# Performance work log

Measured on AMD Instinct MI355X. Metric: run time of the kernel, lower is better.

## Reference

```python
import jax, jax.numpy as jnp
import numpy as np

EMBED_DIM = 768
MAX_LEN = 1024
ALPHA = 0.99
BATCH = 16


def setup_inputs() -> dict:
    key = jax.random.key(0)
    k1, k2, k3 = jax.random.split(key, 3)
    x = jax.random.normal(k1, (BATCH, MAX_LEN, EMBED_DIM), dtype=jnp.float32)
    # torch nn.Linear(embed_dim, 3*embed_dim): store weight as [in, out] for x @ W
    scale = 1.0 / np.sqrt(EMBED_DIM)
    W_qkv = jax.random.uniform(k2, (EMBED_DIM, 3 * EMBED_DIM), dtype=jnp.float32,
                               minval=-scale, maxval=scale)
    b_qkv = jax.random.uniform(k3, (3 * EMBED_DIM,), dtype=jnp.float32,
                               minval=-scale, maxval=scale)
    return {"x": x, "W_qkv": W_qkv, "b_qkv": b_qkv}


def _retention_mask(sl, alpha, dtype):
    # M[i, j] = alpha**(i - j) if i >= j else 0 (causal tril * decay)
    i = jnp.arange(sl)[:, None]
    j = jnp.arange(sl)[None, :]
    causal = i >= j
    # compute decay only where causal to avoid huge alpha**(negative) values
    exponent = jnp.where(causal, (i - j).astype(dtype), 0.0)
    decay = jnp.asarray(alpha, dtype) ** exponent
    return jnp.where(causal, decay, jnp.zeros((), dtype))


def reference(x, W_qkv, b_qkv):
    bs, sl, d = x.shape
    qkv = x @ W_qkv + b_qkv                      # [B, S, 3D]
    q, k, v = jnp.split(qkv, 3, axis=-1)         # each [B, S, D]
    M = _retention_mask(sl, ALPHA, x.dtype)      # [S, S]
    scores = jnp.einsum('bsd,btd->bst', q, k) / jnp.sqrt(jnp.asarray(d, x.dtype))
    out = jnp.einsum('bst,btd->bsd', scores * M[None, :, :], v)
    return out
```

## Files before the change

kernel.cpp:

```cpp
#include <hip/hip_runtime.h>
#include <hip/hip_bf16.h>


#define SEQ   1024
#define DIM   768
#define ND3   2304

typedef __attribute__((ext_vector_type(8))) short bf16x8;
typedef __attribute__((ext_vector_type(4))) float f32x4;

#define L2A     (-0.014499569695115089f)
#define RSQRTD  (0.03608439182435161f)

__device__ __forceinline__ unsigned short f2bf(float x) {
  union { float f; unsigned u; } v; v.f = x;
  unsigned r = v.u + 0x7FFFu + ((v.u >> 16) & 1u);
  return (unsigned short)(r >> 16);
}

__device__ __forceinline__ void gload16(const void* g, void* l) {
  __builtin_amdgcn_global_load_lds(
      (const __attribute__((address_space(1))) void*)g,
      (__attribute__((address_space(3))) void*)l, 16, 0, 0);
}

__device__ __forceinline__ void gemm_core(
    const unsigned short* gA, const unsigned short* gA2,
    const unsigned short* gB, const unsigned short* gB2,
    char* lsA, char* lsB, int nt, int wid, int lane, f32x4 acc[2][4]) {
  int lr = lane & 15, lg = lane >> 4;
  int wm = wid >> 1, wn = wid & 1;
  int rdA = (wm * 32 + lr) * 128 + ((lg ^ (lr & 7)) << 4);
  int rdB = (wn * 64 + lr) * 128 + ((lg ^ (lr & 7)) << 4);
  int wo = wid * 2048;

#define STAGE(t, par) do {                                                    \
    int lo_ = ((par) << 14) + wo;                                             \
    gload16(gA  + (size_t)(t) * 64, lsA + lo_);                               \
    gload16(gA2 + (size_t)(t) * 64, lsA + lo_ + 1024);                        \
    gload16(gB  + (size_t)(t) * 64, lsB + lo_);                               \
    gload16(gB2 + (size_t)(t) * 64, lsB + lo_ + 1024);                        \
  } while (0)

  STAGE(0, 0);
  STAGE(1, 1);
  asm volatile("s_waitcnt vmcnt(4)" ::: "memory");
  __builtin_amdgcn_s_barrier();
  asm volatile("" ::: "memory");

  for (int t = 0; t < nt; ++t) {
    int pbase = (t & 1) << 14;
    bf16x8 aF[2][2], bF[2][4];
#pragma unroll
    for (int kh = 0; kh < 2; ++kh) {
#pragma unroll
      for (int f = 0; f < 2; ++f)
        aF[kh][f] = *(const bf16x8*)(lsA + pbase + ((rdA + f * 2048) ^ (kh << 6)));
#pragma unroll
      for (int n = 0; n < 4; ++n)
        bF[kh][n] = *(const bf16x8*)(lsB + pbase + ((rdB + n * 2048) ^ (kh << 6)));
    }
    __builtin_amdgcn_s_setprio(1);
#pragma unroll
    for (int kh = 0; kh < 2; ++kh)
#pragma unroll
      for (int f = 0; f < 2; ++f)
#pragma unroll
        for (int n = 0; n < 4; ++n)
          acc[f][n] = __builtin_amdgcn_mfma_f32_16x16x32_bf16(aF[kh][f], bF[kh][n], acc[f][n], 0, 0, 0);
    __builtin_amdgcn_s_setprio(0);

    if (t == nt - 1) break;
    __builtin_amdgcn_s_barrier();
    asm volatile("" ::: "memory");
    if (t + 2 < nt) {
      STAGE(t + 2, t & 1);
      asm volatile("s_waitcnt vmcnt(4)" ::: "memory");
    } else {
      asm volatile("s_waitcnt vmcnt(0)" ::: "memory");
    }
    __builtin_amdgcn_s_barrier();
    asm volatile("" ::: "memory");
  }
#undef STAGE
}

__global__ void convert_x(const float* __restrict__ x, unsigned short* __restrict__ xb) {
  size_t i = ((size_t)blockIdx.x * 256 + threadIdx.x) * 8;
  float4 f0 = *(const float4*)(x + i);
  float4 f1 = *(const float4*)(x + i + 4);
  bf16x8 v;
  v[0] = (short)f2bf(f0.x); v[1] = (short)f2bf(f0.y);
  v[2] = (short)f2bf(f0.z); v[3] = (short)f2bf(f0.w);
  v[4] = (short)f2bf(f1.x); v[5] = (short)f2bf(f1.y);
  v[6] = (short)f2bf(f1.z); v[7] = (short)f2bf(f1.w);
  *(bf16x8*)(xb + i) = v;
}

__global__ void transpose_w(const float* __restrict__ W, unsigned short* __restrict__ Wt) {
  __shared__ float tile[64][65];
  int n0 = (blockIdx.x % 36) * 64;
  int k0 = (blockIdx.x / 36) * 64;
  int tx = threadIdx.x & 63, ty = threadIdx.x >> 6;
#pragma unroll
  for (int p = 0; p < 16; ++p) {
    int k = ty + p * 4;
    tile[k][tx] = W[(size_t)(k0 + k) * ND3 + n0 + tx];
  }
  __syncthreads();
#pragma unroll
  for (int p = 0; p < 16; ++p) {
    int n = ty + p * 4;
    Wt[(size_t)(n0 + n) * DIM + k0 + tx] = f2bf(tile[tx][n]);
  }
}

__global__ void __launch_bounds__(512, 4) qkv_g(
    const unsigned short* __restrict__ xb, const unsigned short* __restrict__ Wt,
    const float* __restrict__ bias,
    unsigned short* __restrict__ Qs, unsigned short* __restrict__ Ks,
    unsigned short* __restrict__ Vt) {
  __shared__ char lsA[32768];
  __shared__ char lsB[32768];
  int bid = (blockIdx.x & 7) * 288 + (blockIdx.x >> 3);
  int mt = bid / 18, ntb = bid % 18;
  int m0 = mt * 128, n0 = ntb * 128;

  int tid = threadIdx.x, lane = tid & 63, wid = tid >> 6;
  int l8 = lane >> 3, cs = ((lane & 7) ^ l8) << 3;
  int srow = wid * 16 + l8;

  const unsigned short* gA = xb + (size_t)(m0 + srow) * DIM + cs;
  const unsigned short* gB = Wt + (size_t)(n0 + srow) * DIM + cs;

  f32x4 acc[2][4] = {};
  gemm_core(gA, gA + 8 * DIM, gB, gB + 8 * DIM, lsA, lsB, 12, wid, lane, acc);

  int wm = wid >> 1, wn = wid & 1;
  int lr = lane & 15, lg = lane >> 4;
  float bia[4];
#pragma unroll
  for (int n = 0; n < 4; ++n) bia[n] = bias[n0 + wn * 64 + n * 16 + lr];

  if (ntb < 6) {
#pragma unroll
    for (int f = 0; f < 2; ++f)
#pragma unroll
      for (int r = 0; r < 4; ++r) {
        int mg = m0 + wm * 32 + f * 16 + lg * 4 + r;
        int b = mg >> 10, s = mg & 1023;
        float sc = exp2f((float)s * L2A) * RSQRTD;
        unsigned short* dst = Qs + ((size_t)b * SEQ + s) * DIM + n0 + wn * 64 + lr;
#pragma unroll
        for (int n = 0; n < 4; ++n)
          dst[n * 16] = f2bf((acc[f][n][r] + bia[n]) * sc);
      }
  } else if (ntb < 12) {
#pragma unroll
    for (int f = 0; f < 2; ++f)
#pragma unroll
      for (int r = 0; r < 4; ++r) {
        int mg = m0 + wm * 32 + f * 16 + lg * 4 + r;
        int b = mg >> 10, s = mg & 1023;
        float sc = exp2f(-(float)s * L2A);
        unsigned short* dst = Ks + ((size_t)b * SEQ + s) * DIM + (n0 - DIM) + wn * 64 + lr;
#pragma unroll
        for (int n = 0; n < 4; ++n)
          dst[n * 16] = f2bf((acc[f][n][r] + bia[n]) * sc);
      }
  } else {
#pragma unroll
    for (int f = 0; f < 2; ++f)
#pragma unroll
      for (int r = 0; r < 4; ++r) {
        int mg = m0 + wm * 32 + f * 16 + lg * 4 + r;
        int b = mg >> 10, s = mg & 1023;
        int d = (n0 - 2 * DIM) + wn * 64 + lr;
        unsigned short* dst = Vt + ((size_t)b * DIM + d) * SEQ + s;
#pragma unroll
        for (int n = 0; n < 4; ++n)
          dst[(size_t)n * 16 * SEQ] = f2bf(acc[f][n][r] + bia[n]);
      }
  }
}

__global__ void __launch_bounds__(512, 4) score_g(
    const unsigned short* __restrict__ Qs, const unsigned short* __restrict__ Ks,
    unsigned short* __restrict__ Sm, int b_base) {
  __shared__ char lsA[32768];
  __shared__ char lsB[32768];
  int bid = (blockIdx.x & 7) * (gridDim.x >> 3) + (blockIdx.x >> 3);
  int t = bid % 36, bl = bid / 36;
  int b = b_base + bl;
  int it = 0;
  while (t >= it + 1) { t -= it + 1; it++; }
  int jt = t;
  int m0 = it * 128, n0 = jt * 128;
  const unsigned short* A  = Qs + (size_t)b * SEQ * DIM;
  const unsigned short* Bt = Ks + (size_t)b * SEQ * DIM;
  unsigned short* Smp = Sm + (size_t)bl * SEQ * SEQ;

  int tid = threadIdx.x, lane = tid & 63, wid = tid >> 6;
  int l8 = lane >> 3, cs = ((lane & 7) ^ l8) << 3;
  int srow = wid * 16 + l8;

  const unsigned short* gA = A  + (size_t)(m0 + srow) * DIM + cs;
  const unsigned short* gB = Bt + (size_t)(n0 + srow) * DIM + cs;

  f32x4 acc[2][4] = {};
  gemm_core(gA, gA + 8 * DIM, gB, gB + 8 * DIM, lsA, lsB, 12, wid, lane, acc);

  int wm = wid >> 1, wn = wid & 1;
  int lr = lane & 15, lg = lane >> 4;
#pragma unroll
  for (int f = 0; f < 2; ++f)
#pragma unroll
    for (int n = 0; n < 4; ++n) {
      int j = n0 + wn * 64 + n * 16 + lr;
#pragma unroll
      for (int r = 0; r < 4; ++r) {
        int i = m0 + wm * 32 + f * 16 + lg * 4 + r;
        float v = acc[f][n][r];
        if (j > i) v = 0.0f;
        Smp[(size_t)i * SEQ + j] = f2bf(v);
      }
    }
}

__global__ void __launch_bounds__(512, 4) pv_g(
    const unsigned short* __restrict__ Sm, const unsigned short* __restrict__ Vt,
    float* __restrict__ out, int b_base, int gsz) {
  __shared__ char lsA[32768];
  __shared__ char lsB[32768];
  int it = 7 - blockIdx.x / (gsz * 6);
  int rem = blockIdx.x % (gsz * 6);
  int bl = rem / 6, dt = rem % 6;
  int b = b_base + bl;
  int m0 = it * 128, n0 = dt * 128;
  const unsigned short* A  = Sm + (size_t)bl * SEQ * SEQ;
  const unsigned short* Bt = Vt + (size_t)b * DIM * SEQ;
  int nt = (it + 1) * 2;

  int tid = threadIdx.x, lane = tid & 63, wid = tid >> 6;
  int l8 = lane >> 3, cs = ((lane & 7) ^ l8) << 3;
  int srow = wid * 16 + l8;

  const unsigned short* gA = A  + (size_t)(m0 + srow) * SEQ + cs;
  const unsigned short* gB = Bt + (size_t)(n0 + srow) * SEQ + cs;

  f32x4 acc[2][4] = {};
  gemm_core(gA, gA + 8 * SEQ, gB, gB + 8 * SEQ, lsA, lsB, nt, wid, lane, acc);

  int wm = wid >> 1, wn = wid & 1;
  int lr = lane & 15, lg = lane >> 4;
#pragma unroll
  for (int f = 0; f < 2; ++f)
#pragma unroll
    for (int n = 0; n < 4; ++n) {
      int d = n0 + wn * 64 + n * 16 + lr;
#pragma unroll
      for (int r = 0; r < 4; ++r) {
        int i = m0 + wm * 32 + f * 16 + lg * 4 + r;
        out[((size_t)b * SEQ + i) * DIM + d] = acc[f][n][r];
      }
    }
}

extern "C" void kernel_launch(void* const* d_in, const int* in_sizes, int n_in,
                              void* d_out, int out_size, void* d_ws, size_t ws_size,
                              hipStream_t stream) {
  const float* x    = (const float*)d_in[0];
  const float* W    = (const float*)d_in[1];
  const float* bias = (const float*)d_in[2];
  float* out = (float*)d_out;

  char* ws = (char*)d_ws;
  unsigned short* Wt = (unsigned short*)(ws);
  unsigned short* Qs = (unsigned short*)(ws + 3538944);
  unsigned short* Ks = (unsigned short*)(ws + 3538944 + 25165824);
  unsigned short* Vt = (unsigned short*)(ws + 3538944 + 2 * 25165824);
  unsigned short* Sm = (unsigned short*)(ws + 3538944 + 3 * 25165824);
  unsigned short* xb = (unsigned short*)d_out;

  size_t smBase = 3538944 + 3 * (size_t)25165824;
  int gsz = (ws_size >= smBase + (size_t)16 * SEQ * SEQ * 2) ? 16 : 8;
  int ngrp = 16 / gsz;

  transpose_w<<<36 * 12, 256, 0, stream>>>(W, Wt);
  convert_x<<<6144, 256, 0, stream>>>(x, xb);
  qkv_g<<<2304, 512, 0, stream>>>(xb, Wt, bias, Qs, Ks, Vt);
  for (int g = 0; g < ngrp; ++g) {
    score_g<<<gsz * 36, 512, 0, stream>>>(Qs, Ks, Sm, g * gsz);
    pv_g<<<gsz * 48, 512, 0, stream>>>(Sm, Vt, out, g * gsz, gsz);
  }
}
```

Before: 149.5 us.

## Replace QKV projection GEMM with 256x256-tile 8-wave ping-pong kernel

Swaps the 128x128-tile QKV projection kernel for a new 256x256-tile kernel. It uses 128 KB of double-buffered LDS and an explicitly interleaved schedule of LDS reads, MFMA bursts at raised priority, barriers and vmcnt-gated async global-to-LDS loads. The larger tile raises arithmetic intensity and reduces redundant global traffic, and the hand schedule aims to overlap loads with MFMA work. In exchange it needs a 32-block accumulator per thread (more registers), cuts occupancy to 2 blocks per CU by launch bounds, and launches only 576 blocks, which may underfill the GPU or cause tail effects.

New measurement: 155.7 us. 4.2% more time.

```diff
diff --git a/kernel.cpp b/kernel.cpp
--- a/kernel.cpp
+++ b/kernel.cpp
@@ -23,6 +23,158 @@
       (const __attribute__((address_space(1))) void*)g,
       (__attribute__((address_space(3))) void*)l, 16, 0, 0);
 }
+
+
+__global__ void __launch_bounds__(512, 2) qkv_g8(
+    const unsigned short* __restrict__ xb, const unsigned short* __restrict__ Wt,
+    const float* __restrict__ bias,
+    unsigned short* __restrict__ Qs, unsigned short* __restrict__ Ks,
+    unsigned short* __restrict__ Vt) {
+  __shared__ __align__(1024) char ls[131072];
+  char* lsA = ls;
+  char* lsB = ls + 65536;
+
+  int bid = (blockIdx.x & 7) * 72 + (blockIdx.x >> 3);
+  int mt = bid / 9, ntb = bid % 9;
+  int m0 = mt * 256, n0 = ntb * 256;
+
+  int tid = threadIdx.x, lane = tid & 63, wid = tid >> 6;
+  int wm = wid >> 2, wn = wid & 3;
+  int lr = lane & 15, lg = lane >> 4;
+  int l8 = lane >> 3, cs = ((lane & 7) ^ l8) << 3;
+
+  const unsigned short* pA = xb + (size_t)(m0 + l8) * DIM + cs;
+  const unsigned short* pB = Wt + (size_t)(n0 + l8) * DIM + cs;
+
+  int rdA = wm * 16384 + lr * 128 + ((lg ^ (lr & 7)) << 4);
+  int rdB = (wn >> 1) * 16384 + (wn & 1) * 8192 + lr * 128 + ((lg ^ (lr & 7)) << 4);
+
+#define STG_A(kt, h) do {                                                      \
+    gload16(pA + (size_t)((h) * 128 + wid * 16) * DIM + (kt) * 64,             \
+            lsA + (((kt) & 1) << 15) + ((h) << 14) + wid * 2048);              \
+    gload16(pA + (size_t)((h) * 128 + wid * 16 + 8) * DIM + (kt) * 64,         \
+            lsA + (((kt) & 1) << 15) + ((h) << 14) + wid * 2048 + 1024);       \
+  } while (0)
+#define STG_B(kt, h) do {                                                      \
+    gload16(pB + (size_t)((h) * 128 + wid * 16) * DIM + (kt) * 64,             \
+            lsB + (((kt) & 1) << 15) + ((h) << 14) + wid * 2048);              \
+    gload16(pB + (size_t)((h) * 128 + wid * 16 + 8) * DIM + (kt) * 64,         \
+            lsB + (((kt) & 1) << 15) + ((h) << 14) + wid * 2048 + 1024);       \
+  } while (0)
+#define LD_A(kt, mh, ks) do {                                                  \
+    _Pragma("unroll")                                                          \
+    for (int f = 0; f < 4; ++f)                                                \
+      aF[f] = *(const bf16x8*)(lsA + (((kt) & 1) << 15) +                      \
+              ((rdA + (mh) * 8192 + f * 2048) ^ ((ks) << 6)));                 \
+  } while (0)
+#define LD_B(kt, ks) do {                                                      \
+    _Pragma("unroll")                                                          \
+    for (int n = 0; n < 4; ++n)                                                \
+      bF[n] = *(const bf16x8*)(lsB + (((kt) & 1) << 15) +                      \
+              ((rdB + n * 2048) ^ ((ks) << 6)));                               \
+  } while (0)
+#define MFMA16(mh) do {                                                        \
+    __builtin_amdgcn_s_setprio(1);                                             \
+    _Pragma("unroll")                                                          \
+    for (int f = 0; f < 4; ++f)                                                \
+      _Pragma("unroll")                                                        \
+      for (int n = 0; n < 4; ++n)                                              \
+        acc[(mh) * 4 + f][n] = __builtin_amdgcn_mfma_f32_16x16x32_bf16(        \
+            aF[f], bF[n], acc[(mh) * 4 + f][n], 0, 0, 0);                      \
+    __builtin_amdgcn_s_setprio(0);                                             \
+  } while (0)
+#define BAR do { asm volatile("" ::: "memory");                                \
+    __builtin_amdgcn_s_barrier(); asm volatile("" ::: "memory"); } while (0)
+#define GATE(n) asm volatile("s_waitcnt vmcnt(" #n ")" ::: "memory")
+
+  f32x4 acc[8][4] = {};
+  bf16x8 aF[4], bF[4];
+
+  STG_B(0, 0); STG_B(0, 1); STG_A(0, 0); STG_A(0, 1);
+  STG_B(1, 0); STG_B(1, 1);
+  GATE(4);
+  BAR;
+
+  for (int t = 0; t < 6; ++t) {
+    const int kt0 = 2 * t, kt1 = 2 * t + 1, kt2 = 2 * t + 2, kt3 = 2 * t + 3;
+    LD_B(kt0, 0); LD_A(kt0, 0, 0);
+    STG_A(kt1, 0); STG_A(kt1, 1);
+    BAR; MFMA16(0); BAR;
+    LD_A(kt0, 1, 0);
+    BAR; MFMA16(1); BAR;
+    LD_B(kt0, 1); LD_A(kt0, 0, 1);
+    BAR; MFMA16(0); BAR;
+    LD_A(kt0, 1, 1);
+    if (t < 5) { STG_B(kt2, 0); STG_B(kt2, 1); }
+    BAR; MFMA16(1);
+    if (t < 5) GATE(4); else GATE(0);
+    BAR;
+    LD_B(kt1, 0); LD_A(kt1, 0, 0);
+    if (t < 5) { STG_A(kt2, 0); STG_A(kt2, 1); }
+    BAR; MFMA16(0); BAR;
+    LD_A(kt1, 1, 0);
+    BAR; MFMA16(1); BAR;
+    LD_B(kt1, 1); LD_A(kt1, 0, 1);
+    BAR; MFMA16(0); BAR;
+    LD_A(kt1, 1, 1);
+    if (t < 5) { STG_B(kt3, 0); STG_B(kt3, 1); }
+    BAR; MFMA16(1);
+    if (t < 5) { GATE(4); BAR; }
+  }
+#undef STG_A
+#undef STG_B
+#undef LD_A
+#undef LD_B
+#undef MFMA16
+#undef BAR
+#undef GATE
+
+  float bia[4];
+#pragma unroll
+  for (int n = 0; n < 4; ++n) bia[n] = bias[n0 + wn * 64 + n * 16 + lr];
+
+  if (ntb < 3) {
+#pragma unroll
+    for (int f = 0; f < 8; ++f)
+#pragma unroll
+      for (int r = 0; r < 4; ++r) {
+        int mg = m0 + wm * 128 + f * 16 + lg * 4 + r;
+        int b = mg >> 10, s = mg & 1023;
+        float sc = exp2f((float)s * L2A) * RSQRTD;
+        unsigned short* dst = Qs + ((size_t)b * SEQ + s) * DIM + n0 + wn * 64 + lr;
+#pragma unroll
+        for (int n = 0; n < 4; ++n)
+          dst[n * 16] = f2bf((acc[f][n][r] + bia[n]) * sc);
+      }
+  } else if (ntb < 6) {
+#pragma unroll
+    for (int f = 0; f < 8; ++f)
+#pragma unroll
+      for (int r = 0; r < 4; ++r) {
+        int mg = m0 + wm * 128 + f * 16 + lg * 4 + r;
+        int b = mg >> 10, s = mg & 1023;
+        float sc = exp2f(-(float)s * L2A);
+        unsigned short* dst = Ks + ((size_t)b * SEQ + s) * DIM + (n0 - DIM) + wn * 64 + lr;
+#pragma unroll
+        for (int n = 0; n < 4; ++n)
+          dst[n * 16] = f2bf((acc[f][n][r] + bia[n]) * sc);
+      }
+  } else {
+#pragma unroll
+    for (int f = 0; f < 8; ++f)
+#pragma unroll
+      for (int r = 0; r < 4; ++r) {
+        int mg = m0 + wm * 128 + f * 16 + lg * 4 + r;
+        int b = mg >> 10, s = mg & 1023;
+        int d = (n0 - 2 * DIM) + wn * 64 + lr;
+        unsigned short* dst = Vt + ((size_t)b * DIM + d) * SEQ + s;
+#pragma unroll
+        for (int n = 0; n < 4; ++n)
+          dst[(size_t)n * 16 * SEQ] = f2bf(acc[f][n][r] + bia[n]);
+      }
+  }
+}
+
 
 __device__ __forceinline__ void gemm_core(
     const unsigned short* gA, const unsigned short* gA2,
@@ -115,80 +267,11 @@
   }
 }
 
-__global__ void __launch_bounds__(512, 4) qkv_g(
-    const unsigned short* __restrict__ xb, const unsigned short* __restrict__ Wt,
-    const float* __restrict__ bias,
-    unsigned short* __restrict__ Qs, unsigned short* __restrict__ Ks,
-    unsigned short* __restrict__ Vt) {
-  __shared__ char lsA[32768];
-  __shared__ char lsB[32768];
-  int bid = (blockIdx.x & 7) * 288 + (blockIdx.x >> 3);
-  int mt = bid / 18, ntb = bid % 18;
-  int m0 = mt * 128, n0 = ntb * 128;
-
-  int tid = threadIdx.x, lane = tid & 63, wid = tid >> 6;
-  int l8 = lane >> 3, cs = ((lane & 7) ^ l8) << 3;
-  int srow = wid * 16 + l8;
-
-  const unsigned short* gA = xb + (size_t)(m0 + srow) * DIM + cs;
-  const unsigned short* gB = Wt + (size_t)(n0 + srow) * DIM + cs;
-
-  f32x4 acc[2][4] = {};
-  gemm_core(gA, gA + 8 * DIM, gB, gB + 8 * DIM, lsA, lsB, 12, wid, lane, acc);
-
-  int wm = wid >> 1, wn = wid & 1;
-  int lr = lane & 15, lg = lane >> 4;
-  float bia[4];
-#pragma unroll
-  for (int n = 0; n < 4; ++n) bia[n] = bias[n0 + wn * 64 + n * 16 + lr];
-
-  if (ntb < 6) {
-#pragma unroll
-    for (int f = 0; f < 2; ++f)
-#pragma unroll
-      for (int r = 0; r < 4; ++r) {
-        int mg = m0 + wm * 32 + f * 16 + lg * 4 + r;
-        int b = mg >> 10, s = mg & 1023;
-        float sc = exp2f((float)s * L2A) * RSQRTD;
-        unsigned short* dst = Qs + ((size_t)b * SEQ + s) * DIM + n0 + wn * 64 + lr;
-#pragma unroll
-        for (int n = 0; n < 4; ++n)
-          dst[n * 16] = f2bf((acc[f][n][r] + bia[n]) * sc);
-      }
-  } else if (ntb < 12) {
-#pragma unroll
-    for (int f = 0; f < 2; ++f)
-#pragma unroll
-      for (int r = 0; r < 4; ++r) {
-        int mg = m0 + wm * 32 + f * 16 + lg * 4 + r;
-        int b = mg >> 10, s = mg & 1023;
-        float sc = exp2f(-(float)s * L2A);
-        unsigned short* dst = Ks + ((size_t)b * SEQ + s) * DIM + (n0 - DIM) + wn * 64 + lr;
-#pragma unroll
-        for (int n = 0; n < 4; ++n)
-          dst[n * 16] = f2bf((acc[f][n][r] + bia[n]) * sc);
-      }
-  } else {
-#pragma unroll
-    for (int f = 0; f < 2; ++f)
-#pragma unroll
-      for (int r = 0; r < 4; ++r) {
-        int mg = m0 + wm * 32 + f * 16 + lg * 4 + r;
-        int b = mg >> 10, s = mg & 1023;
-        int d = (n0 - 2 * DIM) + wn * 64 + lr;
-        unsigned short* dst = Vt + ((size_t)b * DIM + d) * SEQ + s;
-#pragma unroll
-        for (int n = 0; n < 4; ++n)
-          dst[(size_t)n * 16 * SEQ] = f2bf(acc[f][n][r] + bia[n]);
-      }
-  }
-}
-
 __global__ void __launch_bounds__(512, 4) score_g(
     const unsigned short* __restrict__ Qs, const unsigned short* __restrict__ Ks,
     unsigned short* __restrict__ Sm, int b_base) {
-  __shared__ char lsA[32768];
-  __shared__ char lsB[32768];
+  __shared__ __align__(1024) char lsA[32768];
+  __shared__ __align__(1024) char lsB[32768];
   int bid = (blockIdx.x & 7) * (gridDim.x >> 3) + (blockIdx.x >> 3);
   int t = bid % 36, bl = bid / 36;
   int b = b_base + bl;
@@ -230,8 +313,8 @@
 __global__ void __launch_bounds__(512, 4) pv_g(
     const unsigned short* __restrict__ Sm, const unsigned short* __restrict__ Vt,
     float* __restrict__ out, int b_base, int gsz) {
-  __shared__ char lsA[32768];
-  __shared__ char lsB[32768];
+  __shared__ __align__(1024) char lsA[32768];
+  __shared__ __align__(1024) char lsB[32768];
   int it = 7 - blockIdx.x / (gsz * 6);
   int rem = blockIdx.x % (gsz * 6);
   int bl = rem / 6, dt = rem % 6;
@@ -288,7 +371,7 @@
 
   transpose_w<<<36 * 12, 256, 0, stream>>>(W, Wt);
   convert_x<<<6144, 256, 0, stream>>>(x, xb);
-  qkv_g<<<2304, 512, 0, stream>>>(xb, Wt, bias, Qs, Ks, Vt);
+  qkv_g8<<<576, 512, 0, stream>>>(xb, Wt, bias, Qs, Ks, Vt);
   for (int g = 0; g < ngrp; ++g) {
     score_g<<<gsz * 36, 512, 0, stream>>>(Qs, Ks, Sm, g * gsz);
     pv_g<<<gsz * 48, 512, 0, stream>>>(Sm, Vt, out, g * gsz, gsz);
```

## Merge prep kernels and retile QKV GEMM to 128x256 with vectorized V stores

Applied to the files above, without the earlier changes.

Merges the x conversion and W transpose into one launch to save a kernel launch. Rewrites the QKV projection GEMM with a dedicated kernel: 128x256 output tiles over 8 waves (each 64x64), K-step of 32 with a new swizzled LDS layout, and half as many blocks. This raises arithmetic intensity per LDS load. V transpose stores now write 4 contiguous bf16 per lane instead of scattered scalar stores. It adds register pressure (64 accumulators) and twice as many K iterations, each carrying barrier overhead.

After: 152.3 us. No clear change (+1.9%).

```diff
diff --git a/kernel.cpp b/kernel.cpp
--- a/kernel.cpp
+++ b/kernel.cpp
@@ -22,6 +22,158 @@
   __builtin_amdgcn_global_load_lds(
       (const __attribute__((address_space(1))) void*)g,
       (__attribute__((address_space(3))) void*)l, 16, 0, 0);
+}
+
+__global__ void prep(const float* __restrict__ x, unsigned short* __restrict__ xb,
+                     const float* __restrict__ W, unsigned short* __restrict__ Wt) {
+  __shared__ float tile[64][65];
+  int bid = blockIdx.x;
+  if (bid < 6144) {
+    size_t i = ((size_t)bid * 256 + threadIdx.x) * 8;
+    float4 f0 = *(const float4*)(x + i);
+    float4 f1 = *(const float4*)(x + i + 4);
+    bf16x8 v;
+    v[0] = (short)f2bf(f0.x); v[1] = (short)f2bf(f0.y);
+    v[2] = (short)f2bf(f0.z); v[3] = (short)f2bf(f0.w);
+    v[4] = (short)f2bf(f1.x); v[5] = (short)f2bf(f1.y);
+    v[6] = (short)f2bf(f1.z); v[7] = (short)f2bf(f1.w);
+    *(bf16x8*)(xb + i) = v;
+  } else {
+    int tb = bid - 6144;
+    int n0 = (tb % 36) * 64;
+    int k0 = (tb / 36) * 64;
+    int tx = threadIdx.x & 63, ty = threadIdx.x >> 6;
+#pragma unroll
+    for (int p = 0; p < 16; ++p) {
+      int k = ty + p * 4;
+      tile[k][tx] = W[(size_t)(k0 + k) * ND3 + n0 + tx];
+    }
+    __syncthreads();
+#pragma unroll
+    for (int p = 0; p < 16; ++p) {
+      int n = ty + p * 4;
+      Wt[(size_t)(n0 + n) * DIM + k0 + tx] = f2bf(tile[tx][n]);
+    }
+  }
+}
+
+__global__ void __launch_bounds__(512, 4) qkv_g(
+    const unsigned short* __restrict__ xb, const unsigned short* __restrict__ Wt,
+    const float* __restrict__ bias,
+    unsigned short* __restrict__ Qs, unsigned short* __restrict__ Ks,
+    unsigned short* __restrict__ Vt) {
+  __shared__ __align__(1024) char lsA[16384];
+  __shared__ __align__(1024) char lsB[32768];
+  int bid = (blockIdx.x & 7) * 144 + (blockIdx.x >> 3);
+  int mt = bid / 9, ntb = bid % 9;
+  int m0 = mt * 128, n0 = ntb * 256;
+
+  int tid = threadIdx.x, lane = tid & 63, wid = tid >> 6;
+  int lr = lane & 15, lg = lane >> 4;
+  int wm = wid >> 2, wn = wid & 3;
+  int c8 = (lane & 7) ^ (lane >> 3);
+  int rloc = (lane >> 3) * 2 + (c8 >> 2), colo = (c8 & 3) * 8;
+  const unsigned short* gA = xb + (size_t)(m0 + rloc) * DIM + colo;
+  const unsigned short* gB = Wt + (size_t)(n0 + rloc) * DIM + colo;
+  int slot16 = (((((lr & 1) << 2) | lg) ^ ((lr >> 1) & 7)) << 4);
+  int rdA = wm * 4096 + (lr >> 1) * 128 + slot16;
+  int rdB = wn * 4096 + (lr >> 1) * 128 + slot16;
+
+  f32x4 acc[4][4] = {};
+
+#define STG(t, par) do {                                                      \
+    char* la_ = lsA + (par) * 8192;                                           \
+    char* lb_ = lsB + (par) * 16384;                                          \
+    gload16(gA + (size_t)(wid * 16) * DIM + (t) * 32, la_ + wid * 1024);      \
+    gload16(gB + (size_t)(wid * 32) * DIM + (t) * 32, lb_ + wid * 2048);      \
+    gload16(gB + (size_t)(wid * 32 + 16) * DIM + (t) * 32,                    \
+            lb_ + wid * 2048 + 1024);                                         \
+  } while (0)
+
+  STG(0, 0);
+  STG(1, 1);
+  asm volatile("s_waitcnt vmcnt(3)" ::: "memory");
+  __builtin_amdgcn_s_barrier();
+  asm volatile("" ::: "memory");
+
+  for (int t = 0; t < 24; ++t) {
+    int pA = (t & 1) * 8192, pB = (t & 1) * 16384;
+    bf16x8 aF[4], bF[4];
+#pragma unroll
+    for (int f = 0; f < 4; ++f)
+      aF[f] = *(const bf16x8*)(lsA + pA + rdA + f * 1024);
+#pragma unroll
+    for (int n = 0; n < 4; ++n)
+      bF[n] = *(const bf16x8*)(lsB + pB + rdB + n * 1024);
+    __builtin_amdgcn_s_setprio(1);
+#pragma unroll
+    for (int f = 0; f < 4; ++f)
+#pragma unroll
+      for (int n = 0; n < 4; ++n)
+        acc[f][n] = __builtin_amdgcn_mfma_f32_16x16x32_bf16(aF[f], bF[n], acc[f][n], 0, 0, 0);
+    __builtin_amdgcn_s_setprio(0);
+
+    if (t == 23) break;
+    __builtin_amdgcn_s_barrier();
+    asm volatile("" ::: "memory");
+    if (t + 2 < 24) {
+      STG(t + 2, t & 1);
+      asm volatile("s_waitcnt vmcnt(3)" ::: "memory");
+    } else {
+      asm volatile("s_waitcnt vmcnt(0)" ::: "memory");
+    }
+    __builtin_amdgcn_s_barrier();
+    asm volatile("" ::: "memory");
+  }
+#undef STG
+
+  float bia[4];
+#pragma unroll
+  for (int n = 0; n < 4; ++n) bia[n] = bias[n0 + wn * 64 + n * 16 + lr];
+
+  if (ntb < 3) {
+#pragma unroll
+    for (int f = 0; f < 4; ++f)
+#pragma unroll
+      for (int r = 0; r < 4; ++r) {
+        int mg = m0 + wm * 64 + f * 16 + lg * 4 + r;
+        int b = mg >> 10, s = mg & 1023;
+        float sc = exp2f((float)s * L2A) * RSQRTD;
+        unsigned short* dst = Qs + ((size_t)b * SEQ + s) * DIM + n0 + wn * 64 + lr;
+#pragma unroll
+        for (int n = 0; n < 4; ++n)
+          dst[n * 16] = f2bf((acc[f][n][r] + bia[n]) * sc);
+      }
+  } else if (ntb < 6) {
+#pragma unroll
+    for (int f = 0; f < 4; ++f)
+#pragma unroll
+      for (int r = 0; r < 4; ++r) {
+        int mg = m0 + wm * 64 + f * 16 + lg * 4 + r;
+        int b = mg >> 10, s = mg & 1023;
+        float sc = exp2f(-(float)s * L2A);
+        unsigned short* dst = Ks + ((size_t)b * SEQ + s) * DIM + (n0 - DIM) + wn * 64 + lr;
+#pragma unroll
+        for (int n = 0; n < 4; ++n)
+          dst[n * 16] = f2bf((acc[f][n][r] + bia[n]) * sc);
+      }
+  } else {
+#pragma unroll
+    for (int f = 0; f < 4; ++f) {
+      int mg = m0 + wm * 64 + f * 16 + lg * 4;
+      int b = mg >> 10, s0 = mg & 1023;
+#pragma unroll
+      for (int n = 0; n < 4; ++n) {
+        int d = (n0 - 2 * DIM) + wn * 64 + n * 16 + lr;
+        ushort4 v;
+        v.x = f2bf(acc[f][n][0] + bia[n]);
+        v.y = f2bf(acc[f][n][1] + bia[n]);
+        v.z = f2bf(acc[f][n][2] + bia[n]);
+        v.w = f2bf(acc[f][n][3] + bia[n]);
+        *(ushort4*)(Vt + ((size_t)b * DIM + d) * SEQ + s0) = v;
+      }
+    }
+  }
 }
 
 __device__ __forceinline__ void gemm_core(
@@ -85,110 +237,11 @@
 #undef STAGE
 }
 
-__global__ void convert_x(const float* __restrict__ x, unsigned short* __restrict__ xb) {
-  size_t i = ((size_t)blockIdx.x * 256 + threadIdx.x) * 8;
-  float4 f0 = *(const float4*)(x + i);
-  float4 f1 = *(const float4*)(x + i + 4);
-  bf16x8 v;
-  v[0] = (short)f2bf(f0.x); v[1] = (short)f2bf(f0.y);
-  v[2] = (short)f2bf(f0.z); v[3] = (short)f2bf(f0.w);
-  v[4] = (short)f2bf(f1.x); v[5] = (short)f2bf(f1.y);
-  v[6] = (short)f2bf(f1.z); v[7] = (short)f2bf(f1.w);
-  *(bf16x8*)(xb + i) = v;
-}
-
-__global__ void transpose_w(const float* __restrict__ W, unsigned short* __restrict__ Wt) {
-  __shared__ float tile[64][65];
-  int n0 = (blockIdx.x % 36) * 64;
-  int k0 = (blockIdx.x / 36) * 64;
-  int tx = threadIdx.x & 63, ty = threadIdx.x >> 6;
-#pragma unroll
-  for (int p = 0; p < 16; ++p) {
-    int k = ty + p * 4;
-    tile[k][tx] = W[(size_t)(k0 + k) * ND3 + n0 + tx];
-  }
-  __syncthreads();
-#pragma unroll
-  for (int p = 0; p < 16; ++p) {
-    int n = ty + p * 4;
-    Wt[(size_t)(n0 + n) * DIM + k0 + tx] = f2bf(tile[tx][n]);
-  }
-}
-
-__global__ void __launch_bounds__(512, 4) qkv_g(
-    const unsigned short* __restrict__ xb, const unsigned short* __restrict__ Wt,
-    const float* __restrict__ bias,
-    unsigned short* __restrict__ Qs, unsigned short* __restrict__ Ks,
-    unsigned short* __restrict__ Vt) {
-  __shared__ char lsA[32768];
-  __shared__ char lsB[32768];
-  int bid = (blockIdx.x & 7) * 288 + (blockIdx.x >> 3);
-  int mt = bid / 18, ntb = bid % 18;
-  int m0 = mt * 128, n0 = ntb * 128;
-
-  int tid = threadIdx.x, lane = tid & 63, wid = tid >> 6;
-  int l8 = lane >> 3, cs = ((lane & 7) ^ l8) << 3;
-  int srow = wid * 16 + l8;
-
-  const unsigned short* gA = xb + (size_t)(m0 + srow) * DIM + cs;
-  const unsigned short* gB = Wt + (size_t)(n0 + srow) * DIM + cs;
-
-  f32x4 acc[2][4] = {};
-  gemm_core(gA, gA + 8 * DIM, gB, gB + 8 * DIM, lsA, lsB, 12, wid, lane, acc);
-
-  int wm = wid >> 1, wn = wid & 1;
-  int lr = lane & 15, lg = lane >> 4;
-  float bia[4];
-#pragma unroll
-  for (int n = 0; n < 4; ++n) bia[n] = bias[n0 + wn * 64 + n * 16 + lr];
-
-  if (ntb < 6) {
-#pragma unroll
-    for (int f = 0; f < 2; ++f)
-#pragma unroll
-      for (int r = 0; r < 4; ++r) {
-        int mg = m0 + wm * 32 + f * 16 + lg * 4 + r;
-        int b = mg >> 10, s = mg & 1023;
-        float sc = exp2f((float)s * L2A) * RSQRTD;
-        unsigned short* dst = Qs + ((size_t)b * SEQ + s) * DIM + n0 + wn * 64 + lr;
-#pragma unroll
-        for (int n = 0; n < 4; ++n)
-          dst[n * 16] = f2bf((acc[f][n][r] + bia[n]) * sc);
-      }
-  } else if (ntb < 12) {
-#pragma unroll
-    for (int f = 0; f < 2; ++f)
-#pragma unroll
-      for (int r = 0; r < 4; ++r) {
-        int mg = m0 + wm * 32 + f * 16 + lg * 4 + r;
-        int b = mg >> 10, s = mg & 1023;
-        float sc = exp2f(-(float)s * L2A);
-        unsigned short* dst = Ks + ((size_t)b * SEQ + s) * DIM + (n0 - DIM) + wn * 64 + lr;
-#pragma unroll
-        for (int n = 0; n < 4; ++n)
-          dst[n * 16] = f2bf((acc[f][n][r] + bia[n]) * sc);
-      }
-  } else {
-#pragma unroll
-    for (int f = 0; f < 2; ++f)
-#pragma unroll
-      for (int r = 0; r < 4; ++r) {
-        int mg = m0 + wm * 32 + f * 16 + lg * 4 + r;
-        int b = mg >> 10, s = mg & 1023;
-        int d = (n0 - 2 * DIM) + wn * 64 + lr;
-        unsigned short* dst = Vt + ((size_t)b * DIM + d) * SEQ + s;
-#pragma unroll
-        for (int n = 0; n < 4; ++n)
-          dst[(size_t)n * 16 * SEQ] = f2bf(acc[f][n][r] + bia[n]);
-      }
-  }
-}
-
 __global__ void __launch_bounds__(512, 4) score_g(
     const unsigned short* __restrict__ Qs, const unsigned short* __restrict__ Ks,
     unsigned short* __restrict__ Sm, int b_base) {
-  __shared__ char lsA[32768];
-  __shared__ char lsB[32768];
+  __shared__ __align__(1024) char lsA[32768];
+  __shared__ __align__(1024) char lsB[32768];
   int bid = (blockIdx.x & 7) * (gridDim.x >> 3) + (blockIdx.x >> 3);
   int t = bid % 36, bl = bid / 36;
   int b = b_base + bl;
@@ -230,8 +283,8 @@
 __global__ void __launch_bounds__(512, 4) pv_g(
     const unsigned short* __restrict__ Sm, const unsigned short* __restrict__ Vt,
     float* __restrict__ out, int b_base, int gsz) {
-  __shared__ char lsA[32768];
-  __shared__ char lsB[32768];
+  __shared__ __align__(1024) char lsA[32768];
+  __shared__ __align__(1024) char lsB[32768];
   int it = 7 - blockIdx.x / (gsz * 6);
   int rem = blockIdx.x % (gsz * 6);
   int bl = rem / 6, dt = rem % 6;
@@ -286,9 +339,8 @@
   int gsz = (ws_size >= smBase + (size_t)16 * SEQ * SEQ * 2) ? 16 : 8;
   int ngrp = 16 / gsz;
 
-  transpose_w<<<36 * 12, 256, 0, stream>>>(W, Wt);
-  convert_x<<<6144, 256, 0, stream>>>(x, xb);
-  qkv_g<<<2304, 512, 0, stream>>>(xb, Wt, bias, Qs, Ks, Vt);
+  prep<<<6576, 256, 0, stream>>>(x, xb, W, Wt);
+  qkv_g<<<1152, 512, 0, stream>>>(xb, Wt, bias, Qs, Ks, Vt);
   for (int g = 0; g < ngrp; ++g) {
     score_g<<<gsz * 36, 512, 0, stream>>>(Qs, Ks, Sm, g * gsz);
     pv_g<<<gsz * 48, 512, 0, stream>>>(Sm, Vt, out, g * gsz, gsz);
```
